# Kernel optimization log

Hardware: AMD Instinct MI355X
Metric: run time of the kernel (lower is better)

The kernel has to match this reference:

```python
import jax, jax.numpy as jnp
import numpy as np

B, S, D, H = 4, 2048, 1024, 16
HD = D // H  # head_dim = 64


def setup_inputs() -> dict:
    key = jax.random.key(0)
    ks = jax.random.split(key, 5)
    s = 1.0 / np.sqrt(D)
    return {
        "x": jax.random.normal(ks[0], (B, S, D), jnp.float32),
        "Wq": jax.random.normal(ks[1], (D, D), jnp.float32) * s,
        "Wk": jax.random.normal(ks[2], (D, D), jnp.float32) * s,
        "Wv": jax.random.normal(ks[3], (D, D), jnp.float32) * s,
        "Wo": jax.random.normal(ks[4], (D, D), jnp.float32) * s,
        "bo": jnp.zeros((D,), jnp.float32),
    }


def reference(x, Wq, Wk, Wv, Wo, bo):
    b, s, d = x.shape
    # projections (torch Linear: x @ W.T; weights here stored as [in, out] equivalent)
    q = (x @ Wq).reshape(b, s, H, HD).transpose(0, 2, 1, 3)  # [b,h,s,hd]
    k = (x @ Wk).reshape(b, s, H, HD).transpose(0, 2, 1, 3)
    v = (x @ Wv).reshape(b, s, H, HD).transpose(0, 2, 1, 3)
    scores = jnp.einsum("bhqd,bhkd->bhqk", q, k) * (HD ** -0.5)
    causal = jnp.tril(jnp.ones((s, s), bool))  # mask==0 -> -inf
    scores = jnp.where(causal, scores, -jnp.inf)
    attn = jax.nn.softmax(scores, axis=-1)
    out = jnp.einsum("bhqk,bhkd->bhqd", attn, v)
    out = out.transpose(0, 2, 1, 3).reshape(b, s, d)
    return out @ Wo + bo
```

## Files before the change

kernel.cpp:

```cpp
#include <hip/hip_runtime.h>
#include <cstdint>
#include <cstddef>

typedef __attribute__((ext_vector_type(8))) short bf16x8;
typedef __attribute__((ext_vector_type(4))) float f32x4;
typedef __attribute__((ext_vector_type(16))) float f32x16;

constexpr int Bsz = 4, Ssz = 2048, Dsz = 1024, Hn = 16, HDsz = 64;
constexpr int Msz = Bsz * Ssz;
constexpr float LOG2E = 1.4426950408889634f;

#define MFMA32(a, b, c) __builtin_amdgcn_mfma_f32_16x16x32_bf16(a, b, c, 0, 0, 0)
#define MFMA3232(a, b, c) __builtin_amdgcn_mfma_f32_32x32x16_bf16(a, b, c, 0, 0, 0)

__device__ __forceinline__ unsigned short f2bf(float f) {
  union { float f; unsigned int u; } v; v.f = f;
  unsigned int r = v.u + 0x7fffu + ((v.u >> 16) & 1u);
  return (unsigned short)(r >> 16);
}

__device__ __forceinline__ int cvtpk(float a, float b) {
  int r;
  asm("v_cvt_pk_bf16_f32 %0, %1, %2" : "=v"(r) : "v"(a), "v"(b));
  return r;
}
__device__ __forceinline__ void pswap(int& a, int& b) {
  asm("v_permlane32_swap_b32 %0, %1" : "+v"(a), "+v"(b));
}

typedef __attribute__((address_space(1))) const unsigned int gu32;
typedef __attribute__((address_space(3))) unsigned int lu32;
__device__ __forceinline__ void async_cp16(const unsigned short* g, unsigned short* l) {
  __builtin_amdgcn_global_load_lds((gu32*)g, (lu32*)l, 16, 0, 0);
}

__global__ void prep_kernel(const float* __restrict__ x, unsigned short* __restrict__ xb,
                            const float* __restrict__ W0, const float* __restrict__ W1,
                            const float* __restrict__ W2, const float* __restrict__ W3,
                            unsigned short* __restrict__ T0, unsigned short* __restrict__ T1,
                            unsigned short* __restrict__ T2, unsigned short* __restrict__ T3) {
  const int z = blockIdx.z;
  if (z == 4) {
    const int i0 = (blockIdx.y * 32 + blockIdx.x) * 2048 + threadIdx.x;
#pragma unroll
    for (int j = 0; j < 8; j++) {
      const int i = i0 + j * 256;
      const float4 v = reinterpret_cast<const float4*>(x)[i];
      ushort4 o;
      o.x = f2bf(v.x); o.y = f2bf(v.y); o.z = f2bf(v.z); o.w = f2bf(v.w);
      reinterpret_cast<ushort4*>(xb)[i] = o;
    }
    return;
  }
  __shared__ float tile[32][33];
  const float* W = (z == 0) ? W0 : (z == 1) ? W1 : (z == 2) ? W2 : W3;
  unsigned short* Wt = (z == 0) ? T0 : (z == 1) ? T1 : (z == 2) ? T2 : T3;
  int tx = threadIdx.x & 31, ty = threadIdx.x >> 5;
  int bx = blockIdx.x, by = blockIdx.y;
#pragma unroll
  for (int i = 0; i < 4; i++) {
    int k = by * 32 + ty + i * 8;
    tile[ty + i * 8][tx] = W[k * Dsz + bx * 32 + tx];
  }
  __syncthreads();
#pragma unroll
  for (int i = 0; i < 4; i++) {
    int nrow = bx * 32 + ty + i * 8;
    Wt[nrow * Dsz + by * 32 + tx] = f2bf(tile[tx][ty + i * 8]);
  }
}

enum { EPI_QKV = 0, EPI_OUT = 1 };

template <int EPI>
__global__ __launch_bounds__(512, 4)
void gemm_bk64(const unsigned short* __restrict__ A,
               const unsigned short* __restrict__ Bt,
               unsigned short* __restrict__ Qh,
               unsigned short* __restrict__ Kh,
               unsigned short* __restrict__ Vth,
               float* __restrict__ Out,
               const float* __restrict__ bias) {
  __shared__ unsigned short As[128 * 64];
  __shared__ unsigned short Bs[128 * 64];

  const int tid = threadIdx.x;
  const int w = tid >> 6, lane = tid & 63;
  const int l15 = lane & 15, quad = lane >> 4;
  const int wr = w >> 1, wc = w & 1;
  const int orig = blockIdx.y * gridDim.x + blockIdx.x;
  const int xcd = orig & 7, idx = orig >> 3;
  const int bm = (xcd << 3) | (idx & 7);
  const int bn = idx >> 3;
  const int rr = lane >> 3;
  const int scoff = ((lane & 7) ^ rr) * 8;

  f32x4 acc[2][4];
#pragma unroll
  for (int i = 0; i < 2; i++)
#pragma unroll
    for (int j = 0; j < 4; j++) acc[i][j] = (f32x4){0.f, 0.f, 0.f, 0.f};

  const int rowA0 = bm * 128, rowB0 = bn * 128;

  for (int kt = 0; kt < Dsz / 64; kt++) {
#pragma unroll
    for (int i = 0; i < 2; i++) {
      const int r8 = w * 16 + i * 8;
      async_cp16(&A[(size_t)(rowA0 + r8 + rr) * Dsz + kt * 64 + scoff], &As[r8 * 64]);
      async_cp16(&Bt[(size_t)(rowB0 + r8 + rr) * Dsz + kt * 64 + scoff], &Bs[r8 * 64]);
    }
    __syncthreads();

#pragma unroll
    for (int ks = 0; ks < 2; ks++) {
      bf16x8 af[2], bfr[4];
#pragma unroll
      for (int t = 0; t < 2; t++) {
        const int ra = wr * 32 + t * 16 + l15;
        af[t] = *reinterpret_cast<const bf16x8*>(
            &As[ra * 64 + (((ks * 4 + quad) ^ (ra & 7)) * 8)]);
      }
#pragma unroll
      for (int t = 0; t < 4; t++) {
        const int rb = wc * 64 + t * 16 + l15;
        bfr[t] = *reinterpret_cast<const bf16x8*>(
            &Bs[rb * 64 + (((ks * 4 + quad) ^ (rb & 7)) * 8)]);
      }
#pragma unroll
      for (int i = 0; i < 2; i++)
#pragma unroll
        for (int j = 0; j < 4; j++)
          acc[i][j] = MFMA32(af[i], bfr[j], acc[i][j]);
    }
    __syncthreads();
  }

  if (EPI == EPI_QKV) {
    const int proj = (bn * 128) >> 10;
#pragma unroll
    for (int i = 0; i < 2; i++) {
#pragma unroll
      for (int j = 0; j < 4; j++) {
        const int n = bn * 128 + wc * 64 + j * 16 + l15;
        const int nn = n & 1023, h = nn >> 6, hd = nn & 63;
        const int m0 = bm * 128 + wr * 32 + i * 16 + quad * 4;
        const int b = m0 >> 11, s0 = m0 & (Ssz - 1);
        if (proj == 0) {
#pragma unroll
          for (int r = 0; r < 4; r++)
            Qh[((size_t)(b * Hn + h) * Ssz + s0 + r) * HDsz + hd] =
                f2bf(acc[i][j][r] * (0.125f * LOG2E));
        } else if (proj == 1) {
#pragma unroll
          for (int r = 0; r < 4; r++)
            Kh[((size_t)(b * Hn + h) * Ssz + s0 + r) * HDsz + hd] = f2bf(acc[i][j][r]);
        } else {
          ushort4 o;
          o.x = f2bf(acc[i][j][0]); o.y = f2bf(acc[i][j][1]);
          o.z = f2bf(acc[i][j][2]); o.w = f2bf(acc[i][j][3]);
          *reinterpret_cast<ushort4*>(
              &Vth[((size_t)(b * Hn + h) * HDsz + hd) * Ssz + s0]) = o;
        }
      }
    }
  } else {
#pragma unroll
    for (int i = 0; i < 2; i++) {
#pragma unroll
      for (int j = 0; j < 4; j++) {
        const int n = bn * 128 + wc * 64 + j * 16 + l15;
        const int m0 = bm * 128 + wr * 32 + i * 16 + quad * 4;
#pragma unroll
        for (int r = 0; r < 4; r++)
          Out[(size_t)(m0 + r) * Dsz + n] = acc[i][j][r] + bias[n];
      }
    }
  }
}

__global__ __launch_bounds__(256, 4)
void flash_kernel(const unsigned short* __restrict__ Q,
                  const unsigned short* __restrict__ Kg,
                  const unsigned short* __restrict__ Vt,
                  unsigned short* __restrict__ AO) {
  __shared__ unsigned short Ks[64 * 64];
  __shared__ unsigned short Vs[64 * 64];

  const int tid = threadIdx.x;
  const int w = tid >> 6, lane = tid & 63;
  const int l31 = lane & 31, hi = lane >> 5;
  const int rr = lane >> 3;

  const int linear = blockIdx.y * 16 + blockIdx.x;
  const int bh = (linear & 7) * 8 + ((linear >> 3) & 7);
  const int g = linear >> 6, gk = g >> 2, ga = g & 3;
  const int t = (gk == 0) ? 15 - ga : (gk == 1) ? 8 + ga : (gk == 2) ? 7 - ga : ga;

  const unsigned short* Qb = Q + (size_t)bh * Ssz * HDsz;
  const unsigned short* Kb = Kg + (size_t)bh * Ssz * HDsz;
  const unsigned short* Vb = Vt + (size_t)bh * HDsz * Ssz;
  const int b = bh / Hn, h = bh % Hn;

  const int hl = (l31 & 7) ^ (((l31 >> 3) & 1) << 2);

  const int rowStart = t * 128 + w * 32;
  const int q = rowStart + l31;

  bf16x8 qf[4];
#pragma unroll
  for (int ks = 0; ks < 4; ks++)
    qf[ks] = *reinterpret_cast<const bf16x8*>(
        &Qb[(size_t)q * HDsz + ks * 16 + hi * 8]);

  f32x16 oacc[2];
#pragma unroll
  for (int ho = 0; ho < 2; ho++)
#pragma unroll
    for (int r = 0; r < 16; r++) oacc[ho][r] = 0.f;
  float lpart = 0.f;

  const int nkb = 2 * t + 2;
  for (int kb = 0; kb < nkb; kb++) {
    const int kv0 = kb * 64;
#pragma unroll
    for (int i = 0; i < 2; i++) {
      const int r8 = w * 16 + i * 8;
      const int sc = (((lane & 7) ^ rr ^ (i << 2))) * 8;
      async_cp16(&Kb[(size_t)(kv0 + r8 + rr) * HDsz + sc], &Ks[r8 * 64]);
      async_cp16(&Vb[(size_t)(r8 + rr) * Ssz + kv0 + sc], &Vs[r8 * 64]);
    }
    __syncthreads();

#pragma unroll
    for (int kt = 0; kt < 2; kt++) {
      const bool skip = (kv0 + kt * 32 >= rowStart + 32);
      if (skip) continue;

      f32x16 st;
#pragma unroll
      for (int r = 0; r < 16; r++) st[r] = 0.f;
#pragma unroll
      for (int ks = 0; ks < 4; ks++) {
        const int row = kt * 32 + l31;
        bf16x8 kf = *reinterpret_cast<const bf16x8*>(
            &Ks[row * 64 + (((ks * 2 + hi) ^ hl) * 8)]);
        st = MFMA3232(kf, qf[ks], st);
      }

      const bool needMask = (kv0 + kt * 32 + 31 > rowStart);
      if (needMask) {
#pragma unroll
        for (int r = 0; r < 16; r++) {
          const int kv = kv0 + kt * 32 + (r & 3) + 8 * (r >> 2) + 4 * hi;
          if (kv > q) st[r] = -1e30f;
        }
      }

      float e[16];
#pragma unroll
      for (int r = 0; r < 16; r++) e[r] = __builtin_amdgcn_exp2f(st[r]);
#pragma unroll
      for (int r = 0; r < 16; r += 4)
        lpart += (e[r] + e[r + 1]) + (e[r + 2] + e[r + 3]);

#pragma unroll
      for (int s = 0; s < 2; s++) {
        int a0 = cvtpk(e[8 * s + 0], e[8 * s + 1]);
        int a1 = cvtpk(e[8 * s + 2], e[8 * s + 3]);
        int b0 = cvtpk(e[8 * s + 4], e[8 * s + 5]);
        int b1 = cvtpk(e[8 * s + 6], e[8 * s + 7]);
        pswap(a0, b0);
        pswap(a1, b1);
        union { int u[4]; bf16x8 v; } pa;
        pa.u[0] = a0; pa.u[1] = a1; pa.u[2] = b0; pa.u[3] = b1;
        const int t16 = kt * 2 + s;
#pragma unroll
        for (int ho = 0; ho < 2; ho++) {
          const int row = ho * 32 + l31;
          bf16x8 vf = *reinterpret_cast<const bf16x8*>(
              &Vs[row * 64 + (((t16 * 2 + hi) ^ hl) * 8)]);
          oacc[ho] = MFMA3232(pa.v, vf, oacc[ho]);
        }
      }
    }
    __syncthreads();
  }

  float lf = lpart + __shfl_xor(lpart, 32);
  float linv[16];
#pragma unroll
  for (int r = 0; r < 16; r++) {
    const int qloc = (r & 3) + 8 * (r >> 2) + 4 * hi;
    union { float f; int i; } cv;
    cv.f = lf;
    cv.i = __builtin_amdgcn_ds_bpermute(qloc * 4, cv.i);
    linv[r] = 1.f / cv.f;
  }
#pragma unroll
  for (int r = 0; r < 16; r++) {
    const int qloc = (r & 3) + 8 * (r >> 2) + 4 * hi;
    const size_t m = (size_t)b * Ssz + rowStart + qloc;
#pragma unroll
    for (int ho = 0; ho < 2; ho++) {
      const int n = h * HDsz + ho * 32 + l31;
      AO[m * Dsz + n] = f2bf(oacc[ho][r] * linv[r]);
    }
  }
}

extern "C" void kernel_launch(void* const* d_in, const int* in_sizes, int n_in,
                              void* d_out, int out_size, void* d_ws, size_t ws_size,
                              hipStream_t stream) {
  const float* x  = (const float*)d_in[0];
  const float* Wq = (const float*)d_in[1];
  const float* Wk = (const float*)d_in[2];
  const float* Wv = (const float*)d_in[3];
  const float* Wo = (const float*)d_in[4];
  const float* bo = (const float*)d_in[5];
  float* out = (float*)d_out;

  unsigned short* xb  = (unsigned short*)d_ws;
  unsigned short* Wqt = xb + (size_t)Msz * Dsz;
  unsigned short* Wkt = Wqt + (size_t)Dsz * Dsz;
  unsigned short* Wvt = Wkt + (size_t)Dsz * Dsz;
  unsigned short* Wot = Wvt + (size_t)Dsz * Dsz;
  unsigned short* Qh  = Wot + (size_t)Dsz * Dsz;
  unsigned short* Kh  = Qh + (size_t)Msz * Dsz;
  unsigned short* Vth = Kh + (size_t)Msz * Dsz;
  unsigned short* AO  = Vth + (size_t)Msz * Dsz;

  prep_kernel<<<dim3(32, 32, 5), 256, 0, stream>>>(
      x, xb, Wq, Wk, Wv, Wo, Wqt, Wkt, Wvt, Wot);

  gemm_bk64<EPI_QKV><<<dim3(3 * Dsz / 128, Msz / 128), 512, 0, stream>>>(
      xb, Wqt, Qh, Kh, Vth, nullptr, nullptr);

  flash_kernel<<<dim3(16, Bsz * Hn), 256, 0, stream>>>(Qh, Kh, Vth, AO);

  gemm_bk64<EPI_OUT><<<dim3(Dsz / 128, Msz / 128), 512, 0, stream>>>(
      AO, Wot, nullptr, nullptr, nullptr, out, bo);
}
```

Baseline: 227.3 us.

## Load 128-wide KV tiles per barrier and raise wave priority around MFMAs

The flash attention loop now stages 128 keys (K tile plus two 64-wide V tiles) per iteration instead of 64, halving the number of block-wide barriers and loop iterations. It also brackets the MFMA sections with s_setprio so waves issuing matrix ops are favored over others doing exp/convert work. The cost is doubled LDS per block (32KB), which may reduce occupancy at 4 blocks per CU, and larger load bursts with no double buffering.

```diff
diff --git a/kernel.cpp b/kernel.cpp
--- a/kernel.cpp
+++ b/kernel.cpp
@@ -184,8 +184,8 @@
                   const unsigned short* __restrict__ Kg,
                   const unsigned short* __restrict__ Vt,
                   unsigned short* __restrict__ AO) {
-  __shared__ unsigned short Ks[64 * 64];
-  __shared__ unsigned short Vs[64 * 64];
+  __shared__ unsigned short Ks[128 * 64];
+  __shared__ unsigned short Vs[2][64 * 64];
 
   const int tid = threadIdx.x;
   const int w = tid >> 6, lane = tid & 63;
@@ -220,67 +220,82 @@
     for (int r = 0; r < 16; r++) oacc[ho][r] = 0.f;
   float lpart = 0.f;
 
-  const int nkb = 2 * t + 2;
+  const int nkb = t + 1;
   for (int kb = 0; kb < nkb; kb++) {
-    const int kv0 = kb * 64;
-#pragma unroll
-    for (int i = 0; i < 2; i++) {
-      const int r8 = w * 16 + i * 8;
-      const int sc = (((lane & 7) ^ rr ^ (i << 2))) * 8;
+    const int kv0 = kb * 128;
+#pragma unroll
+    for (int i = 0; i < 4; i++) {
+      const int r8 = w * 32 + i * 8;
+      const int sc = ((lane & 7) ^ rr ^ ((i & 1) << 2)) * 8;
       async_cp16(&Kb[(size_t)(kv0 + r8 + rr) * HDsz + sc], &Ks[r8 * 64]);
-      async_cp16(&Vb[(size_t)(r8 + rr) * Ssz + kv0 + sc], &Vs[r8 * 64]);
-    }
+    }
+#pragma unroll
+    for (int c = 0; c < 2; c++)
+#pragma unroll
+      for (int i = 0; i < 2; i++) {
+        const int r8 = w * 16 + i * 8;
+        const int sc = ((lane & 7) ^ rr ^ (i << 2)) * 8;
+        async_cp16(&Vb[(size_t)(r8 + rr) * Ssz + kv0 + c * 64 + sc], &Vs[c][r8 * 64]);
+      }
     __syncthreads();
 
 #pragma unroll
-    for (int kt = 0; kt < 2; kt++) {
-      const bool skip = (kv0 + kt * 32 >= rowStart + 32);
-      if (skip) continue;
-
-      f32x16 st;
-#pragma unroll
-      for (int r = 0; r < 16; r++) st[r] = 0.f;
-#pragma unroll
-      for (int ks = 0; ks < 4; ks++) {
-        const int row = kt * 32 + l31;
-        bf16x8 kf = *reinterpret_cast<const bf16x8*>(
-            &Ks[row * 64 + (((ks * 2 + hi) ^ hl) * 8)]);
-        st = MFMA3232(kf, qf[ks], st);
-      }
-
-      const bool needMask = (kv0 + kt * 32 + 31 > rowStart);
-      if (needMask) {
-#pragma unroll
-        for (int r = 0; r < 16; r++) {
-          const int kv = kv0 + kt * 32 + (r & 3) + 8 * (r >> 2) + 4 * hi;
-          if (kv > q) st[r] = -1e30f;
+    for (int half = 0; half < 2; half++) {
+      const int kvh = kv0 + half * 64;
+#pragma unroll
+      for (int kt = 0; kt < 2; kt++) {
+        const bool skip = (kvh + kt * 32 >= rowStart + 32);
+        if (skip) continue;
+
+        f32x16 st;
+#pragma unroll
+        for (int r = 0; r < 16; r++) st[r] = 0.f;
+        __builtin_amdgcn_s_setprio(1);
+#pragma unroll
+        for (int ks = 0; ks < 4; ks++) {
+          const int row = half * 64 + kt * 32 + l31;
+          bf16x8 kf = *reinterpret_cast<const bf16x8*>(
+              &Ks[row * 64 + (((ks * 2 + hi) ^ hl) * 8)]);
+          st = MFMA3232(kf, qf[ks], st);
         }
-      }
-
-      float e[16];
-#pragma unroll
-      for (int r = 0; r < 16; r++) e[r] = __builtin_amdgcn_exp2f(st[r]);
-#pragma unroll
-      for (int r = 0; r < 16; r += 4)
-        lpart += (e[r] + e[r + 1]) + (e[r + 2] + e[r + 3]);
-
-#pragma unroll
-      for (int s = 0; s < 2; s++) {
-        int a0 = cvtpk(e[8 * s + 0], e[8 * s + 1]);
-        int a1 = cvtpk(e[8 * s + 2], e[8 * s + 3]);
-        int b0 = cvtpk(e[8 * s + 4], e[8 * s + 5]);
-        int b1 = cvtpk(e[8 * s + 6], e[8 * s + 7]);
-        pswap(a0, b0);
-        pswap(a1, b1);
-        union { int u[4]; bf16x8 v; } pa;
-        pa.u[0] = a0; pa.u[1] = a1; pa.u[2] = b0; pa.u[3] = b1;
-        const int t16 = kt * 2 + s;
-#pragma unroll
-        for (int ho = 0; ho < 2; ho++) {
-          const int row = ho * 32 + l31;
-          bf16x8 vf = *reinterpret_cast<const bf16x8*>(
-              &Vs[row * 64 + (((t16 * 2 + hi) ^ hl) * 8)]);
-          oacc[ho] = MFMA3232(pa.v, vf, oacc[ho]);
+        __builtin_amdgcn_s_setprio(0);
+
+        const bool needMask = (kvh + kt * 32 + 31 > rowStart);
+        if (needMask) {
+#pragma unroll
+          for (int r = 0; r < 16; r++) {
+            const int kv = kvh + kt * 32 + (r & 3) + 8 * (r >> 2) + 4 * hi;
+            if (kv > q) st[r] = -1e30f;
+          }
+        }
+
+        float e[16];
+#pragma unroll
+        for (int r = 0; r < 16; r++) e[r] = __builtin_amdgcn_exp2f(st[r]);
+#pragma unroll
+        for (int r = 0; r < 16; r += 4)
+          lpart += (e[r] + e[r + 1]) + (e[r + 2] + e[r + 3]);
+
+#pragma unroll
+        for (int s = 0; s < 2; s++) {
+          int a0 = cvtpk(e[8 * s + 0], e[8 * s + 1]);
+          int a1 = cvtpk(e[8 * s + 2], e[8 * s + 3]);
+          int b0 = cvtpk(e[8 * s + 4], e[8 * s + 5]);
+          int b1 = cvtpk(e[8 * s + 6], e[8 * s + 7]);
+          pswap(a0, b0);
+          pswap(a1, b1);
+          union { int u[4]; bf16x8 v; } pa;
+          pa.u[0] = a0; pa.u[1] = a1; pa.u[2] = b0; pa.u[3] = b1;
+          const int t16 = kt * 2 + s;
+          __builtin_amdgcn_s_setprio(1);
+#pragma unroll
+          for (int ho = 0; ho < 2; ho++) {
+            const int row = ho * 32 + l31;
+            bf16x8 vf = *reinterpret_cast<const bf16x8*>(
+                &Vs[half][row * 64 + (((t16 * 2 + hi) ^ hl) * 8)]);
+            oacc[ho] = MFMA3232(pa.v, vf, oacc[ho]);
+          }
+          __builtin_amdgcn_s_setprio(0);
         }
       }
     }
```

New measurement: 223.8 us. About the same (-1.5%).
